# Kernel optimization log

Hardware: AMD Instinct MI355X
Metric: run time of the kernel (lower is better)

## Reference

```python
import jax, jax.numpy as jnp
import numpy as np

B, C, N, K, COUT = 8, 128, 10000, 16, 256


def setup_inputs() -> dict:
    key = jax.random.key(0)
    ks = jax.random.split(key, 8)
    x = jax.random.normal(ks[0], (B, C, N, 1), dtype=jnp.float32)
    edge_index = jax.random.randint(ks[1], (2, B, N, K), 0, N)
    s1 = 1.0 / np.sqrt(C)
    W1 = jax.random.uniform(ks[2], (C, C), jnp.float32, -s1, s1)   # nn1 1x1 conv weight
    b1 = jax.random.uniform(ks[3], (C,), jnp.float32, -s1, s1)
    Wp = jax.random.uniform(ks[4], (C, C), jnp.float32, -s1, s1)   # nn_pooling Linear
    bp = jax.random.uniform(ks[5], (C,), jnp.float32, -s1, s1)
    s2 = 1.0 / np.sqrt(2 * C)
    W2 = jax.random.uniform(ks[6], (COUT, 2 * C), jnp.float32, -s2, s2)  # nn2 1x1 conv
    b2 = jax.random.uniform(ks[7], (COUT,), jnp.float32, -s2, s2)
    return dict(x=x, edge_index=edge_index, W1=W1, b1=b1, Wp=Wp, bp=bp, W2=W2, b2=b2)


def reference(x, edge_index, W1, b1, Wp, bp, W2, b2):
    b, c, n, _ = x.shape
    k = edge_index.shape[-1]
    # nn1: 1x1 conv (channel mix) + ReLU -> [B,C,N,1]
    h = jax.nn.relu(jnp.einsum('bcns,dc->bdns', x, W1) + b1[None, :, None, None])
    # batched_index_select: gather neighbor features along vertex dim -> [B,C,N,K]
    hn = h[:, :, :, 0]                              # [B,C,N]
    idx = edge_index[0].reshape(b, 1, n * k)        # broadcast over C
    xj = jnp.take_along_axis(hn, idx, axis=2).reshape(b, c, n, k)
    # nn_pooling: Linear over channel dim + ReLU (transpose(1,3) in torch == act on C)
    xj = jax.nn.relu(jnp.einsum('bcnk,dc->bdnk', xj, Wp) + bp[None, :, None, None])
    # max-pool over neighbors, keepdim -> [B,C,N,1]
    xj = jnp.max(xj, axis=-1, keepdims=True)
    # concat along channels, nn2: 1x1 conv + ReLU -> [B,COUT,N,1]
    cat = jnp.concatenate([h, xj], axis=1)
    out = jax.nn.relu(jnp.einsum('bcns,dc->bdns', cat, W2) + b2[None, :, None, None])
    return out
```

## Files before the change

### kernel.cpp

```cpp
#include <hip/hip_runtime.h>

#define NODES 10000
#define BATCH 8
#define CH    128
#define KNB   16
#define CO    256

typedef __bf16 bf16x8 __attribute__((ext_vector_type(8)));
typedef float  f32x4  __attribute__((ext_vector_type(4)));

__device__ __forceinline__ unsigned short f2bf(float f) {
  unsigned u = __float_as_uint(f);
  u = (u + 0x7FFFu + ((u >> 16) & 1u)) >> 16;
  return (unsigned short)u;
}

__device__ __forceinline__ unsigned pkmax(unsigned a, unsigned b) {
  unsigned d;
  asm("v_pk_max_u16 %0, %1, %2" : "=v"(d) : "v"(a), "v"(b));
  return d;
}
__device__ __forceinline__ uint4 pkmax4(uint4 a, uint4 b) {
  a.x = pkmax(a.x, b.x); a.y = pkmax(a.y, b.y);
  a.z = pkmax(a.z, b.z); a.w = pkmax(a.w, b.w);
  return a;
}
__device__ __forceinline__ bf16x8 asbf8(uint4 u) {
  union { uint4 u; bf16x8 b; } c; c.u = u; return c.b;
}

__global__ __launch_bounds__(256) void prep(
    const float* __restrict__ W1, const float* __restrict__ Wp,
    const float* __restrict__ W2,
    unsigned short* __restrict__ W1b, unsigned short* __restrict__ Wpb,
    unsigned short* __restrict__ W2b)
{
  int i = blockIdx.x * 256 + threadIdx.x;
  const float* src; unsigned short* dst; int off;
  if (i < 4096)      { src = W1; dst = W1b; off = i; }
  else if (i < 8192) { src = Wp; dst = Wpb; off = i - 4096; }
  else               { src = W2; dst = W2b; off = i - 8192; }
  float4 v = ((const float4*)src)[off];
  ushort4 o;
  o.x = f2bf(v.x); o.y = f2bf(v.y); o.z = f2bf(v.z); o.w = f2bf(v.w);
  ((ushort4*)dst)[off] = o;
}

__global__ __launch_bounds__(256) void fused_hz(
    const unsigned short* __restrict__ W1b, const float* __restrict__ b1,
    const unsigned short* __restrict__ Wpb, const float* __restrict__ bp,
    const float* __restrict__ x,
    unsigned short* __restrict__ h_t, unsigned short* __restrict__ z_t)
{
  const int b  = blockIdx.y;
  const int n0 = blockIdx.x * 64;
  const int t  = threadIdx.x;
  const int lane = t & 63, w = t >> 6;
  const int lm = lane & 15, q = lane >> 4;

  __shared__ __align__(16) unsigned short Bt[64 * 128];
  __shared__ __align__(16) unsigned short Ht[64 * 128];
  char* BtB = (char*)Bt;
  char* HtB = (char*)Ht;

  {
    const float* X = x + (size_t)b * CH * NODES;
#pragma unroll
    for (int rep = 0; rep < 4; ++rep) {
      int flat = t + rep * 256;
      int c2 = flat >> 4, n4 = flat & 15;
      int c  = c2 * 2;
      int gn = n0 + n4 * 4;
      float4 a0 = make_float4(0.f,0.f,0.f,0.f), a1 = a0;
      if (gn < NODES) {
        a0 = *(const float4*)(X + (size_t)c * NODES + gn);
        a1 = *(const float4*)(X + (size_t)(c + 1) * NODES + gn);
      }
      float v0[4] = {a0.x, a0.y, a0.z, a0.w};
      float v1[4] = {a1.x, a1.y, a1.z, a1.w};
#pragma unroll
      for (int i = 0; i < 4; ++i) {
        int nn = n4 * 4 + i;
        unsigned pk = (unsigned)f2bf(v0[i]) | ((unsigned)f2bf(v1[i]) << 16);
        int phys = nn * 256 + (((c2 >> 2) ^ (nn & 7)) << 4) + ((c2 & 3) << 2);
        *(unsigned*)(BtB + phys) = pk;
      }
    }
  }

  const int d0  = (w & 1) * 64;
  const int nbw = (w >> 1) * 32;

  uint4 af[4][4];
#pragma unroll
  for (int dt = 0; dt < 4; ++dt)
#pragma unroll
    for (int kt = 0; kt < 4; ++kt)
      af[dt][kt] = *(const uint4*)(W1b + (d0 + dt*16 + lm) * CH + kt*32 + q*8);

  __syncthreads();

  f32x4 acc[4][2];
#pragma unroll
  for (int dt = 0; dt < 4; ++dt)
#pragma unroll
    for (int nt = 0; nt < 2; ++nt) acc[dt][nt] = (f32x4){0.f,0.f,0.f,0.f};

#pragma unroll
  for (int kt = 0; kt < 4; ++kt)
#pragma unroll
    for (int nt = 0; nt < 2; ++nt) {
      int nl = nbw + nt * 16 + lm;
      int chunk = kt * 4 + q;
      int phys = nl * 256 + ((chunk ^ (nl & 7)) << 4);
      bf16x8 bb = asbf8(*(const uint4*)(BtB + phys));
#pragma unroll
      for (int dt = 0; dt < 4; ++dt)
        acc[dt][nt] = __builtin_amdgcn_mfma_f32_16x16x32_bf16(
            asbf8(af[dt][kt]), bb, acc[dt][nt], 0, 0, 0);
    }

  uint4 af2[4][4];
#pragma unroll
  for (int dt = 0; dt < 4; ++dt)
#pragma unroll
    for (int kt = 0; kt < 4; ++kt)
      af2[dt][kt] = *(const uint4*)(Wpb + (d0 + dt*16 + lm) * CH + kt*32 + q*8);

#pragma unroll
  for (int dt = 0; dt < 4; ++dt) {
    int dbase = d0 + dt * 16 + q * 4;
    float4 bi = *(const float4*)(b1 + dbase);
    float bv[4] = {bi.x, bi.y, bi.z, bi.w};
#pragma unroll
    for (int nt = 0; nt < 2; ++nt) {
      int nl = nbw + nt * 16 + lm;
      int gn = n0 + nl;
      ushort4 o;
      o.x = f2bf(fmaxf(acc[dt][nt][0] + bv[0], 0.f));
      o.y = f2bf(fmaxf(acc[dt][nt][1] + bv[1], 0.f));
      o.z = f2bf(fmaxf(acc[dt][nt][2] + bv[2], 0.f));
      o.w = f2bf(fmaxf(acc[dt][nt][3] + bv[3], 0.f));
      int chunk = dbase >> 3;
      int phys  = nl * 256 + ((chunk ^ (nl & 7)) << 4) + ((q & 1) << 3);
      *(ushort4*)(HtB + phys) = o;
      if (gn < NODES)
        *(ushort4*)(h_t + ((size_t)b * NODES + gn) * CH + dbase) = o;
    }
  }

  __syncthreads();

#pragma unroll
  for (int dt = 0; dt < 4; ++dt)
#pragma unroll
    for (int nt = 0; nt < 2; ++nt) acc[dt][nt] = (f32x4){0.f,0.f,0.f,0.f};

#pragma unroll
  for (int kt = 0; kt < 4; ++kt)
#pragma unroll
    for (int nt = 0; nt < 2; ++nt) {
      int nl = nbw + nt * 16 + lm;
      int chunk = kt * 4 + q;
      int phys = nl * 256 + ((chunk ^ (nl & 7)) << 4);
      bf16x8 bb = asbf8(*(const uint4*)(HtB + phys));
#pragma unroll
      for (int dt = 0; dt < 4; ++dt)
        acc[dt][nt] = __builtin_amdgcn_mfma_f32_16x16x32_bf16(
            asbf8(af2[dt][kt]), bb, acc[dt][nt], 0, 0, 0);
    }

#pragma unroll
  for (int dt = 0; dt < 4; ++dt) {
    int dbase = d0 + dt * 16 + q * 4;
    float4 bi = *(const float4*)(bp + dbase);
    float bv[4] = {bi.x, bi.y, bi.z, bi.w};
#pragma unroll
    for (int nt = 0; nt < 2; ++nt) {
      int gn = n0 + nbw + nt * 16 + lm;
      if (gn < NODES) {
        ushort4 o;
        o.x = f2bf(fmaxf(acc[dt][nt][0] + bv[0], 0.f));
        o.y = f2bf(fmaxf(acc[dt][nt][1] + bv[1], 0.f));
        o.z = f2bf(fmaxf(acc[dt][nt][2] + bv[2], 0.f));
        o.w = f2bf(fmaxf(acc[dt][nt][3] + bv[3], 0.f));
        *(ushort4*)(z_t + ((size_t)b * NODES + gn) * CH + dbase) = o;
      }
    }
  }
}

__global__ __launch_bounds__(256) void out_kernel(
    const unsigned short* __restrict__ h_t, const unsigned short* __restrict__ z_t,
    const int* __restrict__ e0, const unsigned short* __restrict__ W2b,
    const float* __restrict__ b2, float* __restrict__ out)
{
  const int bid = blockIdx.x;
  const int b   = bid & 7;
  const int n0  = (bid >> 3) * 64;
  const int t   = threadIdx.x;
  const int lane = t & 63, w = t >> 6;
  const int lm = lane & 15, q = lane >> 4;

  __shared__ __align__(16) unsigned short cat[64 * 256];
  __shared__ __align__(16) int idxs[64 * KNB];
  char* catB = (char*)cat;

  {
    int nl = t >> 2, jq = t & 3;
    int gn = n0 + nl; if (gn > NODES - 1) gn = NODES - 1;
    uint4 iv = *(const uint4*)(e0 + ((size_t)b * NODES + gn) * KNB + jq * 4);
    *(uint4*)&idxs[nl * KNB + jq * 4] = iv;
  }
  __syncthreads();

  {
    const int nl = t >> 2, c = t & 3;
    const char* Z = (const char*)z_t + (size_t)b * NODES * CH * 2 + c * 16;
    uint4 m[4];
#pragma unroll
    for (int cg = 0; cg < 4; ++cg) m[cg] = make_uint4(0u, 0u, 0u, 0u);
#pragma unroll
    for (int k = 0; k < KNB; ++k) {
      int jn = idxs[nl * KNB + k];
      const char* p = Z + (size_t)jn * (CH * 2);
#pragma unroll
      for (int cg = 0; cg < 4; ++cg)
        m[cg] = pkmax4(m[cg], *(const uint4*)(p + cg * 64));
    }
#pragma unroll
    for (int cg = 0; cg < 4; ++cg) {
      int chunk = 16 + cg * 4 + c;
      int phys = nl * 512 + ((chunk ^ (nl & 7)) << 4);
      *(uint4*)(catB + phys) = m[cg];
    }
  }

  {
    const unsigned short* H = h_t + (size_t)b * NODES * CH;
#pragma unroll
    for (int rep = 0; rep < 4; ++rep) {
      int flat = t + rep * 256;
      int nl = flat >> 4, k16 = flat & 15;
      int gn = n0 + nl;
      uint4 v = make_uint4(0u, 0u, 0u, 0u);
      if (gn < NODES) v = *(const uint4*)(H + (size_t)gn * CH + k16 * 8);
      int phys = nl * 512 + ((k16 ^ (nl & 7)) << 4);
      *(uint4*)(catB + phys) = v;
    }
  }

  __syncthreads();

  const int d0 = w * 64;
  f32x4 acc[4][4];
#pragma unroll
  for (int dt = 0; dt < 4; ++dt)
#pragma unroll
    for (int nt = 0; nt < 4; ++nt) acc[dt][nt] = (f32x4){0.f, 0.f, 0.f, 0.f};

  uint4 acur[4], anxt[4];
#pragma unroll
  for (int dt = 0; dt < 4; ++dt)
    acur[dt] = *(const uint4*)(W2b + (d0 + dt * 16 + lm) * CO + q * 8);

#pragma unroll
  for (int kt = 0; kt < 8; ++kt) {
    if (kt < 7) {
#pragma unroll
      for (int dt = 0; dt < 4; ++dt)
        anxt[dt] = *(const uint4*)(W2b + (d0 + dt * 16 + lm) * CO
                                   + (kt + 1) * 32 + q * 8);
    }
#pragma unroll
    for (int nt = 0; nt < 4; ++nt) {
      int nl = nt * 16 + lm;
      int chunk = kt * 4 + q;
      int phys = nl * 512 + ((chunk ^ (nl & 7)) << 4);
      bf16x8 bb = asbf8(*(const uint4*)(catB + phys));
#pragma unroll
      for (int dt = 0; dt < 4; ++dt)
        acc[dt][nt] = __builtin_amdgcn_mfma_f32_16x16x32_bf16(
            asbf8(acur[dt]), bb, acc[dt][nt], 0, 0, 0);
    }
#pragma unroll
    for (int dt = 0; dt < 4; ++dt) acur[dt] = anxt[dt];
  }

#pragma unroll
  for (int dt = 0; dt < 4; ++dt) {
    int dbase = d0 + dt * 16 + q * 4;
    float4 bi = *(const float4*)(b2 + dbase);
    float bv[4] = {bi.x, bi.y, bi.z, bi.w};
#pragma unroll
    for (int nt = 0; nt < 4; ++nt) {
      int gn = n0 + nt * 16 + lm;
      if (gn < NODES) {
        float* op = out + ((size_t)(b * CO + dbase) * NODES) + gn;
#pragma unroll
        for (int r = 0; r < 4; ++r)
          op[(size_t)r * NODES] = fmaxf(acc[dt][nt][r] + bv[r], 0.f);
      }
    }
  }
}

extern "C" void kernel_launch(void* const* d_in, const int* in_sizes, int n_in,
                              void* d_out, int out_size, void* d_ws, size_t ws_size,
                              hipStream_t stream) {
  const float* x  = (const float*)d_in[0];
  const int*   ei = (const int*)d_in[1];
  const float* W1 = (const float*)d_in[2];
  const float* b1 = (const float*)d_in[3];
  const float* Wp = (const float*)d_in[4];
  const float* bp = (const float*)d_in[5];
  const float* W2 = (const float*)d_in[6];
  const float* b2 = (const float*)d_in[7];
  float* out = (float*)d_out;

  unsigned short* ws  = (unsigned short*)d_ws;
  unsigned short* h_t = ws;
  unsigned short* z_t = h_t + (size_t)BATCH * NODES * CH;
  unsigned short* W1b = z_t + (size_t)BATCH * NODES * CH;
  unsigned short* Wpb = W1b + CH * CH;
  unsigned short* W2b = Wpb + CH * CH;

  prep<<<96, 256, 0, stream>>>(W1, Wp, W2, W1b, Wpb, W2b);

  const int NT = (NODES + 63) / 64;
  fused_hz<<<dim3(NT, BATCH), 256, 0, stream>>>(W1b, b1, Wpb, bp, x, h_t, z_t);
  out_kernel<<<BATCH * NT, 256, 0, stream>>>(h_t, z_t, ei, W2b, b2, out);
}
```

Baseline: 205.5 us.

## Split gather-max out of output GEMM kernel into separate pass

Moves the neighbor gather and max over K out of the output GEMM kernel into its own kernel, which writes the pooled features to a new workspace buffer. The GEMM kernel then only stages h and the pooled features into shared memory and drops the index staging and one barrier. The goal is to free the GEMM kernel's register and shared-memory budget and let the latency-bound gather run at higher occupancy. In exchange it costs an extra kernel launch and a full write and read of the pooled tensor through global memory.

```diff
diff --git a/kernel.cpp b/kernel.cpp
--- a/kernel.cpp
+++ b/kernel.cpp
@@ -190,10 +190,51 @@
   }
 }
 
-__global__ __launch_bounds__(256) void out_kernel(
-    const unsigned short* __restrict__ h_t, const unsigned short* __restrict__ z_t,
-    const int* __restrict__ e0, const unsigned short* __restrict__ W2b,
-    const float* __restrict__ b2, float* __restrict__ out)
+__global__ __launch_bounds__(256) void gmax_kernel(
+    const unsigned short* __restrict__ z_t, const int* __restrict__ e0,
+    unsigned short* __restrict__ zm)
+{
+  const int bid = blockIdx.x;
+  const int b   = bid & 7;
+  const int n0  = (bid >> 3) * 64;
+  const int t   = threadIdx.x;
+  const int nl  = t >> 2, c = t & 3;
+  const int gn  = n0 + nl;
+  if (gn >= NODES) return;
+
+  const int* ip = e0 + ((size_t)b * NODES + gn) * KNB;
+  int4 iv0 = *(const int4*)(ip);
+  int4 iv1 = *(const int4*)(ip + 4);
+  int4 iv2 = *(const int4*)(ip + 8);
+  int4 iv3 = *(const int4*)(ip + 12);
+  int idx[16] = {iv0.x, iv0.y, iv0.z, iv0.w,
+                 iv1.x, iv1.y, iv1.z, iv1.w,
+                 iv2.x, iv2.y, iv2.z, iv2.w,
+                 iv3.x, iv3.y, iv3.z, iv3.w};
+
+  const char* Z = (const char*)(z_t + (size_t)b * NODES * CH) + c * 16;
+  uint4 m[4];
+#pragma unroll
+  for (int cg = 0; cg < 4; ++cg) m[cg] = make_uint4(0u, 0u, 0u, 0u);
+
+#pragma unroll
+  for (int k = 0; k < KNB; ++k) {
+    const char* p = Z + (size_t)idx[k] * (CH * 2);
+#pragma unroll
+    for (int cg = 0; cg < 4; ++cg)
+      m[cg] = pkmax4(m[cg], *(const uint4*)(p + cg * 64));
+  }
+
+  char* O = (char*)(zm + ((size_t)b * NODES + gn) * CH) + c * 16;
+#pragma unroll
+  for (int cg = 0; cg < 4; ++cg)
+    *(uint4*)(O + cg * 64) = m[cg];
+}
+
+__global__ __launch_bounds__(256) void out_gemm(
+    const unsigned short* __restrict__ h_t, const unsigned short* __restrict__ zm,
+    const unsigned short* __restrict__ W2b, const float* __restrict__ b2,
+    float* __restrict__ out)
 {
   const int bid = blockIdx.x;
   const int b   = bid & 7;
@@ -203,53 +244,23 @@
   const int lm = lane & 15, q = lane >> 4;
 
   __shared__ __align__(16) unsigned short cat[64 * 256];
-  __shared__ __align__(16) int idxs[64 * KNB];
   char* catB = (char*)cat;
 
-  {
-    int nl = t >> 2, jq = t & 3;
-    int gn = n0 + nl; if (gn > NODES - 1) gn = NODES - 1;
-    uint4 iv = *(const uint4*)(e0 + ((size_t)b * NODES + gn) * KNB + jq * 4);
-    *(uint4*)&idxs[nl * KNB + jq * 4] = iv;
-  }
-  __syncthreads();
-
-  {
-    const int nl = t >> 2, c = t & 3;
-    const char* Z = (const char*)z_t + (size_t)b * NODES * CH * 2 + c * 16;
-    uint4 m[4];
-#pragma unroll
-    for (int cg = 0; cg < 4; ++cg) m[cg] = make_uint4(0u, 0u, 0u, 0u);
-#pragma unroll
-    for (int k = 0; k < KNB; ++k) {
-      int jn = idxs[nl * KNB + k];
-      const char* p = Z + (size_t)jn * (CH * 2);
-#pragma unroll
-      for (int cg = 0; cg < 4; ++cg)
-        m[cg] = pkmax4(m[cg], *(const uint4*)(p + cg * 64));
-    }
-#pragma unroll
-    for (int cg = 0; cg < 4; ++cg) {
-      int chunk = 16 + cg * 4 + c;
-      int phys = nl * 512 + ((chunk ^ (nl & 7)) << 4);
-      *(uint4*)(catB + phys) = m[cg];
-    }
-  }
-
-  {
-    const unsigned short* H = h_t + (size_t)b * NODES * CH;
-#pragma unroll
-    for (int rep = 0; rep < 4; ++rep) {
-      int flat = t + rep * 256;
-      int nl = flat >> 4, k16 = flat & 15;
-      int gn = n0 + nl;
-      uint4 v = make_uint4(0u, 0u, 0u, 0u);
-      if (gn < NODES) v = *(const uint4*)(H + (size_t)gn * CH + k16 * 8);
-      int phys = nl * 512 + ((k16 ^ (nl & 7)) << 4);
-      *(uint4*)(catB + phys) = v;
-    }
-  }
-
+#pragma unroll
+  for (int rep = 0; rep < 8; ++rep) {
+    int flat = t + rep * 256;
+    int nl = flat >> 5, chunk = flat & 31;
+    int gn = n0 + nl;
+    uint4 v = make_uint4(0u, 0u, 0u, 0u);
+    if (gn < NODES) {
+      const unsigned short* src = (chunk < 16)
+        ? h_t + ((size_t)b * NODES + gn) * CH + chunk * 8
+        : zm  + ((size_t)b * NODES + gn) * CH + (chunk - 16) * 8;
+      v = *(const uint4*)src;
+    }
+    int phys = nl * 512 + ((chunk ^ (nl & 7)) << 4);
+    *(uint4*)(catB + phys) = v;
+  }
   __syncthreads();
 
   const int d0 = w * 64;
@@ -324,10 +335,12 @@
   unsigned short* W1b = z_t + (size_t)BATCH * NODES * CH;
   unsigned short* Wpb = W1b + CH * CH;
   unsigned short* W2b = Wpb + CH * CH;
+  unsigned short* zm  = W2b + CO * 2 * CH;
 
   prep<<<96, 256, 0, stream>>>(W1, Wp, W2, W1b, Wpb, W2b);
 
   const int NT = (NODES + 63) / 64;
   fused_hz<<<dim3(NT, BATCH), 256, 0, stream>>>(W1b, b1, Wpb, bp, x, h_t, z_t);
-  out_kernel<<<BATCH * NT, 256, 0, stream>>>(h_t, z_t, ei, W2b, b2, out);
-}
+  gmax_kernel<<<BATCH * NT, 256, 0, stream>>>(z_t, ei, zm);
+  out_gemm<<<BATCH * NT, 256, 0, stream>>>(h_t, zm, W2b, b2, out);
+}
```

Result: no change. 207.8 us (+1.1%).
